# Performance work log

Hardware: AMD Instinct MI355X
Metric: run time of the kernel (lower is better)

The kernel has to match this reference:

```python
import jax, jax.numpy as jnp
import numpy as np

N, E, D, H, O = 100000, 1600000, 256, 128, 64


def setup_inputs() -> dict:
    key = jax.random.key(0)
    ks = jax.random.split(key, 10)
    x = jax.random.normal(ks[0], (N, D), dtype=jnp.float32)
    # edges without self loops (original adds remaining self loops itself)
    row = jax.random.randint(ks[1], (E,), 0, N)
    off = jax.random.randint(ks[2], (E,), 1, N)
    col = (row + off) % N
    edge_index = jnp.stack([row, col]).astype(jnp.int64)
    # positive PPMI edge weights (stand-in for cached random-walk PPMI values)
    ppmi_edge_weight = jax.random.uniform(ks[3], (E,), dtype=jnp.float32, minval=0.1, maxval=1.0)
    # glorot-style weights (shared between GCN and PPMI branches, as in the module)
    W1 = jax.random.normal(ks[4], (D, H), dtype=jnp.float32) * np.sqrt(2.0 / (D + H))
    b1 = jnp.zeros((H,), dtype=jnp.float32)
    W2 = jax.random.normal(ks[5], (H, O), dtype=jnp.float32) * np.sqrt(2.0 / (H + O))
    b2 = jnp.zeros((O,), dtype=jnp.float32)
    dense_w = jax.random.normal(ks[6], (O, 1), dtype=jnp.float32) * np.sqrt(2.0 / (O + 1))
    dense_b = jnp.zeros((1,), dtype=jnp.float32)
    return {"x": x, "edge_index": edge_index, "ppmi_edge_weight": ppmi_edge_weight,
            "W1": W1, "b1": b1, "W2": W2, "b2": b2,
            "dense_w": dense_w, "dense_b": dense_b}


def _sym_norm(row, col, ew, n):
    # deg^-0.5[row] * w * deg^-0.5[col], deg from scatter-add over source index
    deg = jax.ops.segment_sum(ew, row, num_segments=n)
    dis = jnp.where(deg > 0, deg ** -0.5, 0.0)
    return dis[row] * ew * dis[col]


def _gconv(h, W, b, row, col, norm, n):
    hw = h @ W                              # [N, F_out]
    msg = norm[:, None] * hw[row]           # gather + scale, [E', F_out]
    return jax.ops.segment_sum(msg, col, num_segments=n) + b


def reference(x, edge_index, ppmi_edge_weight, W1, b1, W2, b2, dense_w, dense_b):
    n = x.shape[0]
    row = edge_index[0].astype(jnp.int32)
    col = edge_index[1].astype(jnp.int32)
    sl = jnp.arange(n, dtype=jnp.int32)
    row_sl = jnp.concatenate([row, sl])
    col_sl = jnp.concatenate([col, sl])
    ones_sl = jnp.ones((n,), dtype=x.dtype)

    # GCN branch: edge_weight = 1, plus self loops (fill_value = 1)
    gcn_ew = jnp.concatenate([jnp.ones((row.shape[0],), dtype=x.dtype), ones_sl])
    gnorm = _sym_norm(row_sl, col_sl, gcn_ew, n)
    g = jax.nn.relu(_gconv(x, W1, b1, row_sl, col_sl, gnorm, n))  # dropout p in eval -> identity
    g = _gconv(g, W2, b2, row_sl, col_sl, gnorm, n)

    # PPMI branch: precomputed positive weights, plus self loops
    ppmi_ew = jnp.concatenate([ppmi_edge_weight.astype(x.dtype), ones_sl])
    pnorm = _sym_norm(row_sl, col_sl, ppmi_ew, n)
    p = jax.nn.relu(_gconv(x, W1, b1, row_sl, col_sl, pnorm, n))
    p = _gconv(p, W2, b2, row_sl, col_sl, pnorm, n)

    stacked = jnp.stack([g, p], axis=1)                 # [N, 2, O]
    logits = stacked @ dense_w + dense_b                # [N, 2, 1]
    w = jax.nn.softmax(logits, axis=1)
    return jnp.sum(stacked * w, axis=1)                 # [N, O]
```

## Files before the change

### kernel.cpp

```cpp
#include <hip/hip_runtime.h>
#include <hip/hip_bf16.h>
#include <math.h>

#define DD 256
#define HH 128
#define OO 64

#define EPB 8192
#define BKT 512
#define AWIN 512

typedef __attribute__((ext_vector_type(8))) __bf16 bf16x8;
typedef __attribute__((ext_vector_type(4))) __bf16 bf16x4;
typedef __attribute__((ext_vector_type(4))) float f32x4;
typedef __attribute__((ext_vector_type(2))) float f32x2;
typedef __attribute__((ext_vector_type(4))) int i32x4;

__device__ inline float2 bf2_to_f2(unsigned u) {
    float2 r;
    r.x = __uint_as_float(u << 16);
    r.y = __uint_as_float(u & 0xffff0000u);
    return r;
}

__global__ void part_count_kernel(const int* __restrict__ row, const int* __restrict__ col,
                                  int e, int nb,
                                  int* __restrict__ cnt_col, int* __restrict__ cnt_row) {
    __shared__ int hc[256], hr[256];
    int t = threadIdx.x;
    if (t < 256) { hc[t] = 0; hr[t] = 0; }
    __syncthreads();
    int base = blockIdx.x * EPB;
    int lim  = min(EPB, e - base);
    for (int i = t; i < lim; i += 512) {
        atomicAdd(&hc[col[base + i] >> 9], 1);
        atomicAdd(&hr[row[base + i] >> 9], 1);
    }
    __syncthreads();
    if (t < nb) {
        cnt_col[blockIdx.x * nb + t] = hc[t];
        cnt_row[blockIdx.x * nb + t] = hr[t];
    }
}

__global__ void scan_blocks_kernel(const int* __restrict__ cnt_col, const int* __restrict__ cnt_row,
                                   int* __restrict__ base_col, int* __restrict__ base_row,
                                   int* __restrict__ tot_col, int* __restrict__ tot_row,
                                   int nblk, int nb) {
    __shared__ int s[256];
    int side = (blockIdx.x >= (unsigned)nb) ? 1 : 0;
    int b = blockIdx.x - side * nb;
    const int* cnt = side ? cnt_row : cnt_col;
    int* base = side ? base_row : base_col;
    int* tot  = side ? tot_row  : tot_col;
    int t = threadIdx.x;
    int v = (t < nblk) ? cnt[(size_t)t * nb + b] : 0;
    s[t] = v;
    __syncthreads();
    for (int off = 1; off < 256; off <<= 1) {
        int u = (t >= off) ? s[t - off] : 0;
        __syncthreads();
        s[t] += u;
        __syncthreads();
    }
    if (t < nblk) base[(size_t)t * nb + b] = s[t] - v;
    if (t == 255) tot[b] = s[255];
}

__global__ void add_bases_kernel(int* __restrict__ base_col, int* __restrict__ base_row,
                                 const int* __restrict__ tot_col, const int* __restrict__ tot_row,
                                 int* __restrict__ bb_col, int* __restrict__ bb_row,
                                 int* __restrict__ row_ptr, int n, int e, int nblk, int nb) {
    __shared__ int s[256];
    __shared__ int bbv;
    int side = (blockIdx.x >= (unsigned)nb) ? 1 : 0;
    int b = blockIdx.x - side * nb;
    const int* tot = side ? tot_row : tot_col;
    int* base = side ? base_row : base_col;
    int t = threadIdx.x;
    int v = (t < nb) ? tot[t] : 0;
    s[t] = v;
    __syncthreads();
    for (int off = 1; off < 256; off <<= 1) {
        int u = (t >= off) ? s[t - off] : 0;
        __syncthreads();
        s[t] += u;
        __syncthreads();
    }
    if (t == 0) {
        bbv = (b > 0) ? s[b - 1] : 0;
        (side ? bb_row : bb_col)[b] = bbv;
    }
    __syncthreads();
    int add = bbv;
    for (int j = t; j < nblk; j += blockDim.x) base[(size_t)j * nb + b] += add;
    if (blockIdx.x == 0 && t == 0) row_ptr[n] = e;
}

__global__ void part_scatter_kernel(const int* __restrict__ row, const int* __restrict__ col,
                                    const float* __restrict__ ppmi,
                                    const int* __restrict__ base_col, const int* __restrict__ base_row,
                                    int4* __restrict__ tmp_col, int2* __restrict__ tmp_row,
                                    int e, int nb) {
    __shared__ int cc[256], cr[256];
    int t = threadIdx.x;
    if (t < nb) {
        cc[t] = base_col[blockIdx.x * nb + t];
        cr[t] = base_row[blockIdx.x * nb + t];
    }
    __syncthreads();
    int base = blockIdx.x * EPB;
    int lim  = min(EPB, e - base);
    for (int i = t; i < lim; i += 512) {
        int r = row[base + i], c = col[base + i];
        int w = __float_as_int(ppmi[base + i]);
        int sc = atomicAdd(&cc[c >> 9], 1);
        tmp_col[sc] = make_int4(c, r, w, 0);
        int sr = atomicAdd(&cr[r >> 9], 1);
        tmp_row[sr] = make_int2(r, w);
    }
}

__global__ void deg_bucket_kernel(const int2* __restrict__ tmp_row,
                                  const int* __restrict__ bb_row, const int* __restrict__ tot_row,
                                  float2* __restrict__ dis, int n) {
    __shared__ float dg[BKT], dp[BKT];
    int t = threadIdx.x;
    dg[t] = 1.0f; dp[t] = 1.0f;
    __syncthreads();
    int b = blockIdx.x;
    int beg = bb_row[b], cnt = tot_row[b];
    for (int i = t; i < cnt; i += 512) {
        int2 cell = tmp_row[beg + i];
        int lr = cell.x & (BKT - 1);
        atomicAdd(&dg[lr], 1.0f);
        atomicAdd(&dp[lr], __int_as_float(cell.y));
    }
    __syncthreads();
    int g = (b << 9) + t;
    if (g < n) dis[g] = make_float2(rsqrtf(dg[t]), rsqrtf(dp[t]));
}

__launch_bounds__(512)
__global__ void csr_bucket_kernel(const int4* __restrict__ tmp_col,
                                  const int* __restrict__ bb_col, const int* __restrict__ tot_col,
                                  const float2* __restrict__ dis,
                                  int* __restrict__ row_ptr, int4* __restrict__ csr_meta, int n) {
    __shared__ int hist[BKT], s[BKT], cur[BKT];
    int t = threadIdx.x;
    hist[t] = 0;
    __syncthreads();
    int b = blockIdx.x;
    int beg = bb_col[b], cnt = tot_col[b];
    for (int i = t; i < cnt; i += BKT) atomicAdd(&hist[tmp_col[beg + i].x & (BKT - 1)], 1);
    __syncthreads();
    int own = hist[t];
    s[t] = own;
    __syncthreads();
    for (int off = 1; off < BKT; off <<= 1) {
        int v = (t >= off) ? s[t - off] : 0;
        __syncthreads();
        s[t] += v;
        __syncthreads();
    }
    int gslot = beg + s[t] - own;
    cur[t] = gslot;
    int gc = (b << 9) + t;
    if (gc < n) row_ptr[gc] = gslot;
    __syncthreads();
    for (int i = t; i < cnt; i += BKT) {
        int4 cell = tmp_col[beg + i];
        int lc = cell.x & (BKT - 1);
        int slot = atomicAdd(&cur[lc], 1);
        int r = cell.y;
        float w = __int_as_float(cell.z);
        float2 d = dis[r];
        csr_meta[slot] = make_int4(r, __float_as_int(d.x), __float_as_int(d.y * w), 0);
    }
}

__global__ void conv_w_kernel(const float* __restrict__ W, __bf16* __restrict__ Bh,
                              __bf16* __restrict__ Bl, int K, int N) {
    int i = blockIdx.x * blockDim.x + threadIdx.x;
    if (i >= K * N) return;
    int k = i / N, nn = i % N;
    float v = W[i];
    __bf16 h = (__bf16)v;
    Bh[(size_t)nn * K + k] = h;
    Bl[(size_t)nn * K + k] = (__bf16)(v - (float)h);
}

template<int BM, int BN, typename OT, bool ILV>
__launch_bounds__(256, 2)
__global__ void mfma_gemm_kernel(const float* __restrict__ A,
                                 const __bf16* __restrict__ Bth, const __bf16* __restrict__ Btl,
                                 OT* __restrict__ C, int M, int K, int nHalf) {
    constexpr int BK  = 32;
    constexpr int LDK = BK + 8;
    constexpr int WM  = BM / 4;
    constexpr int MT  = WM / 16;
    constexpr int NT  = BN / 16;
    __shared__ __bf16 Ash[BM * LDK];
    __shared__ __bf16 Asl[BM * LDK];
    __shared__ __bf16 Bsh[BN * LDK];
    __shared__ __bf16 Bsl[BN * LDK];

    const int tid  = threadIdx.x;
    const int wave = tid >> 6;
    const int lane = tid & 63;
    const int quad = lane >> 4;
    const int l16  = lane & 15;
    const int row0 = blockIdx.x * BM;

    f32x4 acc[MT][NT] = {};

    for (int k0 = 0; k0 < K; k0 += BK) {
#pragma unroll
        for (int p = 0; p < BM / 32; ++p) {
            int lin = p * 256 + tid;
            int r   = lin >> 3;
            int kc  = (lin & 7) * 4;
            int gr  = row0 + r;
            float4 v;
            if (gr < M) v = *(const float4*)(A + (size_t)gr * K + k0 + kc);
            else        v = make_float4(0.f, 0.f, 0.f, 0.f);
            __bf16 h0 = (__bf16)v.x, h1 = (__bf16)v.y, h2 = (__bf16)v.z, h3 = (__bf16)v.w;
            __bf16 l0 = (__bf16)(v.x - (float)h0), l1 = (__bf16)(v.y - (float)h1);
            __bf16 l2 = (__bf16)(v.z - (float)h2), l3 = (__bf16)(v.w - (float)h3);
            *(bf16x4*)&Ash[r * LDK + kc] = (bf16x4){h0, h1, h2, h3};
            *(bf16x4*)&Asl[r * LDK + kc] = (bf16x4){l0, l1, l2, l3};
        }
#pragma unroll
        for (int p = 0; p < BN / 64; ++p) {
            int lin = p * 256 + tid;
            int r   = lin >> 2;
            int kc  = (lin & 3) * 8;
            *(uint4*)&Bsh[r * LDK + kc] = *(const uint4*)(Bth + (size_t)r * K + k0 + kc);
            *(uint4*)&Bsl[r * LDK + kc] = *(const uint4*)(Btl + (size_t)r * K + k0 + kc);
        }
        __syncthreads();

        bf16x8 bh[NT], bl[NT];
#pragma unroll
        for (int j = 0; j < NT; ++j) {
            bh[j] = *(const bf16x8*)&Bsh[(j * 16 + l16) * LDK + quad * 8];
            bl[j] = *(const bf16x8*)&Bsl[(j * 16 + l16) * LDK + quad * 8];
        }
#pragma unroll
        for (int i = 0; i < MT; ++i) {
            int m = wave * WM + i * 16 + l16;
            bf16x8 ah = *(const bf16x8*)&Ash[m * LDK + quad * 8];
            bf16x8 al = *(const bf16x8*)&Asl[m * LDK + quad * 8];
#pragma unroll
            for (int j = 0; j < NT; ++j) {
                acc[i][j] = __builtin_amdgcn_mfma_f32_16x16x32_bf16(ah, bh[j], acc[i][j], 0, 0, 0);
                acc[i][j] = __builtin_amdgcn_mfma_f32_16x16x32_bf16(ah, bl[j], acc[i][j], 0, 0, 0);
                acc[i][j] = __builtin_amdgcn_mfma_f32_16x16x32_bf16(al, bh[j], acc[i][j], 0, 0, 0);
            }
        }
        __syncthreads();
    }

#pragma unroll
    for (int i = 0; i < MT; ++i) {
#pragma unroll
        for (int rg = 0; rg < 4; ++rg) {
            int gr = row0 + wave * WM + i * 16 + quad * 4 + rg;
            if (gr < M) {
                if constexpr (ILV) {
                    int s = (gr >= nHalf) ? 1 : 0;
                    size_t base = (size_t)(gr - s * nHalf) * (BN * 2) + s;
#pragma unroll
                    for (int j = 0; j < NT; ++j)
                        C[base + (size_t)(j * 16 + l16) * 2] = (OT)acc[i][j][rg];
                } else {
#pragma unroll
                    for (int j = 0; j < NT; ++j)
                        C[(size_t)gr * BN + j * 16 + l16] = (OT)acc[i][j][rg];
                }
            }
        }
    }
}

__global__ void agg1_pull_kernel(const int* __restrict__ row_ptr, const int4* __restrict__ meta,
                                 const __bf16* __restrict__ hw1,
                                 const float2* __restrict__ dis,
                                 const float* __restrict__ b1,
                                 float* __restrict__ g_out, float* __restrict__ p_out, int n) {
    __shared__ i32x4 sm[AWIN];
    const int tid  = threadIdx.x;
    const int wave = tid >> 6;
    const int lane = tid & 63;
    const int c0   = blockIdx.x * 4;
    const int c    = c0 + wave;
    const int beg0 = row_ptr[c0];
    const int end3 = row_ptr[min(c0 + 4, n)];
    int beg = 0, end = 0;
    if (c < n) { beg = row_ptr[c]; end = row_ptr[c + 1]; }
    const int f2 = lane * 2;
    float sgx = 0.f, sgy = 0.f, spx = 0.f, spy = 0.f;

    for (int w = beg0; w < end3; w += AWIN) {
        const int cnt = min(AWIN, end3 - w);
        __syncthreads();
        for (int i = tid; i < cnt; i += 256)
            sm[i] = __builtin_nontemporal_load((const i32x4*)meta + w + i);
        __syncthreads();
        int t = max(beg, w);
        const int hi = min(end, w + cnt);
        for (; t + 8 <= hi; t += 8) {
            i32x4 m[8];
#pragma unroll
            for (int q = 0; q < 8; ++q) m[q] = sm[t - w + q];
            unsigned u[8];
#pragma unroll
            for (int q = 0; q < 8; ++q)
                u[q] = *(const unsigned*)(hw1 + ((size_t)(unsigned)m[q].x << 7) + f2);
#pragma unroll
            for (int q = 0; q < 8; ++q) {
                float2 h = bf2_to_f2(u[q]);
                float wg = __uint_as_float((unsigned)m[q].y);
                float wp = __uint_as_float((unsigned)m[q].z);
                sgx += wg * h.x; sgy += wg * h.y;
                spx += wp * h.x; spy += wp * h.y;
            }
        }
        if (t + 4 <= hi) {
            i32x4 m[4];
#pragma unroll
            for (int q = 0; q < 4; ++q) m[q] = sm[t - w + q];
            unsigned u[4];
#pragma unroll
            for (int q = 0; q < 4; ++q)
                u[q] = *(const unsigned*)(hw1 + ((size_t)(unsigned)m[q].x << 7) + f2);
#pragma unroll
            for (int q = 0; q < 4; ++q) {
                float2 h = bf2_to_f2(u[q]);
                float wg = __uint_as_float((unsigned)m[q].y);
                float wp = __uint_as_float((unsigned)m[q].z);
                sgx += wg * h.x; sgy += wg * h.y;
                spx += wp * h.x; spy += wp * h.y;
            }
            t += 4;
        }
        for (; t < hi; ++t) {
            i32x4 m0 = sm[t - w];
            float2 h0 = bf2_to_f2(*(const unsigned*)(hw1 + ((size_t)(unsigned)m0.x << 7) + f2));
            float wg0 = __uint_as_float((unsigned)m0.y);
            float wp0 = __uint_as_float((unsigned)m0.z);
            sgx += wg0 * h0.x; sgy += wg0 * h0.y;
            spx += wp0 * h0.x; spy += wp0 * h0.y;
        }
    }

    if (c < n) {
        float2 d = dis[c];
        size_t idx = ((size_t)c << 7) + f2;
        float2 hs = bf2_to_f2(*(const unsigned*)(hw1 + idx));
        float2 bv = *(const float2*)(b1 + f2);
        float gx = d.x * sgx + d.x * d.x * hs.x + bv.x;
        float gy = d.x * sgy + d.x * d.x * hs.y + bv.y;
        float px = d.y * spx + d.y * d.y * hs.x + bv.x;
        float py = d.y * spy + d.y * d.y * hs.y + bv.y;
        f32x2 go, po;
        go[0] = gx > 0.f ? gx : 0.f;  go[1] = gy > 0.f ? gy : 0.f;
        po[0] = px > 0.f ? px : 0.f;  po[1] = py > 0.f ? py : 0.f;
        __builtin_nontemporal_store(go, (f32x2*)(g_out + idx));
        __builtin_nontemporal_store(po, (f32x2*)(p_out + idx));
    }
}

__global__ void agg2_final_kernel(const int* __restrict__ row_ptr, const int4* __restrict__ meta,
                                  const __bf16* __restrict__ hw2i,
                                  const float2* __restrict__ dis,
                                  const float* __restrict__ b2,
                                  const float* __restrict__ dense_w, const float* __restrict__ dense_b,
                                  float* __restrict__ out, int n) {
    __shared__ i32x4 sm[AWIN];
    const int tid  = threadIdx.x;
    const int wave = tid >> 6;
    const int f    = tid & 63;
    const int c0   = blockIdx.x * 4;
    const int c    = c0 + wave;
    const int beg0 = row_ptr[c0];
    const int end3 = row_ptr[min(c0 + 4, n)];
    int beg = 0, end = 0;
    if (c < n) { beg = row_ptr[c]; end = row_ptr[c + 1]; }
    const int f2 = f * 2;
    float sg = 0.f, sp = 0.f;

    for (int w = beg0; w < end3; w += AWIN) {
        const int cnt = min(AWIN, end3 - w);
        __syncthreads();
        for (int i = tid; i < cnt; i += 256)
            sm[i] = __builtin_nontemporal_load((const i32x4*)meta + w + i);
        __syncthreads();
        int t = max(beg, w);
        const int hi = min(end, w + cnt);
        for (; t + 8 <= hi; t += 8) {
            i32x4 m[8];
#pragma unroll
            for (int q = 0; q < 8; ++q) m[q] = sm[t - w + q];
            unsigned u[8];
#pragma unroll
            for (int q = 0; q < 8; ++q)
                u[q] = *(const unsigned*)(hw2i + ((size_t)(unsigned)m[q].x << 7) + f2);
#pragma unroll
            for (int q = 0; q < 8; ++q) {
                float2 g0 = bf2_to_f2(u[q]);
                sg += __uint_as_float((unsigned)m[q].y) * g0.x;
                sp += __uint_as_float((unsigned)m[q].z) * g0.y;
            }
        }
        if (t + 4 <= hi) {
            i32x4 m[4];
#pragma unroll
            for (int q = 0; q < 4; ++q) m[q] = sm[t - w + q];
            unsigned u[4];
#pragma unroll
            for (int q = 0; q < 4; ++q)
                u[q] = *(const unsigned*)(hw2i + ((size_t)(unsigned)m[q].x << 7) + f2);
#pragma unroll
            for (int q = 0; q < 4; ++q) {
                float2 g0 = bf2_to_f2(u[q]);
                sg += __uint_as_float((unsigned)m[q].y) * g0.x;
                sp += __uint_as_float((unsigned)m[q].z) * g0.y;
            }
            t += 4;
        }
        for (; t < hi; ++t) {
            i32x4 m0 = sm[t - w];
            float2 g0 = bf2_to_f2(*(const unsigned*)(hw2i + ((size_t)(unsigned)m0.x << 7) + f2));
            sg += __uint_as_float((unsigned)m0.y) * g0.x;
            sp += __uint_as_float((unsigned)m0.z) * g0.y;
        }
    }

    if (c < n) {
        float2 d = dis[c];
        float2 gps = bf2_to_f2(*(const unsigned*)(hw2i + ((size_t)c << 7) + f2));
        float bb = b2[f];
        float gv = d.x * sg + d.x * d.x * gps.x + bb;
        float pv = d.y * sp + d.y * d.y * gps.y + bb;
        float dwv = dense_w[f];
        float lg = gv * dwv, lp = pv * dwv;
#pragma unroll
        for (int off = 32; off > 0; off >>= 1) {
            lg += __shfl_xor(lg, off, 64);
            lp += __shfl_xor(lp, off, 64);
        }
        lg += dense_b[0];
        lp += dense_b[0];
        float m  = fmaxf(lg, lp);
        float eg = expf(lg - m), ep = expf(lp - m);
        float wgt = eg / (eg + ep);
        __builtin_nontemporal_store(wgt * gv + (1.0f - wgt) * pv, out + (size_t)c * OO + f);
    }
}

extern "C" void kernel_launch(void* const* d_in, const int* in_sizes, int n_in,
                              void* d_out, int out_size, void* d_ws, size_t ws_size,
                              hipStream_t stream) {
    const float* x    = (const float*)d_in[0];
    const int*   ei   = (const int*)d_in[1];
    const float* ppmi = (const float*)d_in[2];
    const float* W1   = (const float*)d_in[3];
    const float* b1   = (const float*)d_in[4];
    const float* W2   = (const float*)d_in[5];
    const float* b2   = (const float*)d_in[6];
    const float* dw   = (const float*)d_in[7];
    const float* db   = (const float*)d_in[8];
    float* out = (float*)d_out;

    const int n = in_sizes[0] / DD;
    const int e = in_sizes[2];
    const int* row = ei;
    const int* col = ei + e;

    const int nb   = (n + BKT - 1) / BKT;
    const int nblk = (e + EPB - 1) / EPB;

    float* ws      = (float*)d_ws;
    float2* dis    = (float2*)ws;
    __bf16* hw1    = (__bf16*)(ws + 2 * (size_t)n);
    float* g1      = (float*)(hw1 + (size_t)n * HH);
    float* p1      = g1 + (size_t)n * HH;
    int4* csr_meta = (int4*)(p1 + (size_t)n * HH);
    __bf16* bt1h   = (__bf16*)(csr_meta + e);
    __bf16* bt1l   = bt1h + (size_t)DD * HH;
    __bf16* bt2h   = bt1l + (size_t)DD * HH;
    __bf16* bt2l   = bt2h + (size_t)HH * OO;
    int* row_ptr   = (int*)(bt2l + (size_t)HH * OO);
    int* cnt_col   = row_ptr + (n + 1);
    int* base_col  = cnt_col + (size_t)nblk * nb;
    int* cnt_row   = base_col + (size_t)nblk * nb;
    int* base_row  = cnt_row + (size_t)nblk * nb;
    int* bb_col    = base_row + (size_t)nblk * nb;
    int* tot_col   = bb_col + nb;
    int* bb_row    = tot_col + nb;
    int* tot_row   = bb_row + nb;
    int4* tmp_col  = (int4*)g1;
    int2* tmp_row  = (int2*)p1;
    __bf16* hw2i   = hw1;

    const int T = 256;

    part_count_kernel<<<nblk, 512, 0, stream>>>(row, col, e, nb, cnt_col, cnt_row);
    scan_blocks_kernel<<<2 * nb, T, 0, stream>>>(cnt_col, cnt_row, base_col, base_row,
                                                 tot_col, tot_row, nblk, nb);
    add_bases_kernel<<<2 * nb, T, 0, stream>>>(base_col, base_row, tot_col, tot_row,
                                               bb_col, bb_row, row_ptr, n, e, nblk, nb);
    part_scatter_kernel<<<nblk, 512, 0, stream>>>(row, col, ppmi, base_col, base_row,
                                                  tmp_col, tmp_row, e, nb);
    deg_bucket_kernel<<<nb, 512, 0, stream>>>(tmp_row, bb_row, tot_row, dis, n);
    csr_bucket_kernel<<<nb, BKT, 0, stream>>>(tmp_col, bb_col, tot_col, dis,
                                              row_ptr, csr_meta, n);

    conv_w_kernel<<<(DD * HH + T - 1) / T, T, 0, stream>>>(W1, bt1h, bt1l, DD, HH);
    conv_w_kernel<<<(HH * OO + T - 1) / T, T, 0, stream>>>(W2, bt2h, bt2l, HH, OO);

    mfma_gemm_kernel<128, HH, __bf16, false><<<(n + 127) / 128, 256, 0, stream>>>(
        x, bt1h, bt1l, hw1, n, DD, 0);
    agg1_pull_kernel<<<(n + 3) / 4, 256, 0, stream>>>(row_ptr, csr_meta, hw1, dis, b1, g1, p1, n);
    mfma_gemm_kernel<128, OO, __bf16, true><<<(2 * n + 127) / 128, 256, 0, stream>>>(
        g1, bt2h, bt2l, hw2i, 2 * n, HH, n);
    agg2_final_kernel<<<(n + 3) / 4, 256, 0, stream>>>(row_ptr, csr_meta, hw2i, dis,
                                                       b2, dw, db, out, n);
}
```

Baseline: 512.8 us.

## Load GEMM operands directly into registers, dropping LDS staging and barriers

The split-bf16 MFMA GEMM no longer stages A and B tiles through shared memory. Each wave now loads its own A rows and the B fragments straight from global memory into registers, converts A to hi/lo bf16 in registers, and runs the MFMAs with no __syncthreads. This removes LDS traffic and block-level barriers. In exchange, every wave re-reads the full B fragments from global/L2, and the A loads are strided per lane rather than fully coalesced.

After: 549.2 us. 1.07x slower.

```diff
diff --git a/kernel.cpp b/kernel.cpp
--- a/kernel.cpp
+++ b/kernel.cpp
@@ -190,67 +190,48 @@
     Bl[(size_t)nn * K + k] = (__bf16)(v - (float)h);
 }
 
-template<int BM, int BN, typename OT, bool ILV>
+template<int BN, typename OT, bool ILV>
 __launch_bounds__(256, 2)
-__global__ void mfma_gemm_kernel(const float* __restrict__ A,
-                                 const __bf16* __restrict__ Bth, const __bf16* __restrict__ Btl,
-                                 OT* __restrict__ C, int M, int K, int nHalf) {
-    constexpr int BK  = 32;
-    constexpr int LDK = BK + 8;
-    constexpr int WM  = BM / 4;
-    constexpr int MT  = WM / 16;
-    constexpr int NT  = BN / 16;
-    __shared__ __bf16 Ash[BM * LDK];
-    __shared__ __bf16 Asl[BM * LDK];
-    __shared__ __bf16 Bsh[BN * LDK];
-    __shared__ __bf16 Bsl[BN * LDK];
-
+__global__ void mfma_gemm_reg_kernel(const float* __restrict__ A,
+                                     const __bf16* __restrict__ Bth, const __bf16* __restrict__ Btl,
+                                     OT* __restrict__ C, int M, int K, int nHalf) {
+    constexpr int NT = BN / 16;
     const int tid  = threadIdx.x;
     const int wave = tid >> 6;
     const int lane = tid & 63;
     const int quad = lane >> 4;
     const int l16  = lane & 15;
-    const int row0 = blockIdx.x * BM;
-
-    f32x4 acc[MT][NT] = {};
-
-    for (int k0 = 0; k0 < K; k0 += BK) {
-#pragma unroll
-        for (int p = 0; p < BM / 32; ++p) {
-            int lin = p * 256 + tid;
-            int r   = lin >> 3;
-            int kc  = (lin & 7) * 4;
-            int gr  = row0 + r;
-            float4 v;
-            if (gr < M) v = *(const float4*)(A + (size_t)gr * K + k0 + kc);
-            else        v = make_float4(0.f, 0.f, 0.f, 0.f);
-            __bf16 h0 = (__bf16)v.x, h1 = (__bf16)v.y, h2 = (__bf16)v.z, h3 = (__bf16)v.w;
-            __bf16 l0 = (__bf16)(v.x - (float)h0), l1 = (__bf16)(v.y - (float)h1);
-            __bf16 l2 = (__bf16)(v.z - (float)h2), l3 = (__bf16)(v.w - (float)h3);
-            *(bf16x4*)&Ash[r * LDK + kc] = (bf16x4){h0, h1, h2, h3};
-            *(bf16x4*)&Asl[r * LDK + kc] = (bf16x4){l0, l1, l2, l3};
-        }
-#pragma unroll
-        for (int p = 0; p < BN / 64; ++p) {
-            int lin = p * 256 + tid;
-            int r   = lin >> 2;
-            int kc  = (lin & 3) * 8;
-            *(uint4*)&Bsh[r * LDK + kc] = *(const uint4*)(Bth + (size_t)r * K + k0 + kc);
-            *(uint4*)&Bsl[r * LDK + kc] = *(const uint4*)(Btl + (size_t)r * K + k0 + kc);
-        }
-        __syncthreads();
-
+    const int row0 = blockIdx.x * 128 + wave * 32;
+
+    f32x4 acc[2][NT] = {};
+
+    for (int k0 = 0; k0 < K; k0 += 32) {
         bf16x8 bh[NT], bl[NT];
 #pragma unroll
         for (int j = 0; j < NT; ++j) {
-            bh[j] = *(const bf16x8*)&Bsh[(j * 16 + l16) * LDK + quad * 8];
-            bl[j] = *(const bf16x8*)&Bsl[(j * 16 + l16) * LDK + quad * 8];
-        }
-#pragma unroll
-        for (int i = 0; i < MT; ++i) {
-            int m = wave * WM + i * 16 + l16;
-            bf16x8 ah = *(const bf16x8*)&Ash[m * LDK + quad * 8];
-            bf16x8 al = *(const bf16x8*)&Asl[m * LDK + quad * 8];
+            size_t boff = (size_t)(j * 16 + l16) * K + k0 + quad * 8;
+            bh[j] = *(const bf16x8*)(Bth + boff);
+            bl[j] = *(const bf16x8*)(Btl + boff);
+        }
+#pragma unroll
+        for (int i = 0; i < 2; ++i) {
+            int gr = row0 + i * 16 + l16;
+            float4 v0 = make_float4(0.f, 0.f, 0.f, 0.f);
+            float4 v1 = make_float4(0.f, 0.f, 0.f, 0.f);
+            if (gr < M) {
+                const float* ap = A + (size_t)gr * K + k0 + quad * 8;
+                v0 = *(const float4*)ap;
+                v1 = *(const float4*)(ap + 4);
+            }
+            float vv0 = v0.x, vv1 = v0.y, vv2 = v0.z, vv3 = v0.w;
+            float vv4 = v1.x, vv5 = v1.y, vv6 = v1.z, vv7 = v1.w;
+            __bf16 h0 = (__bf16)vv0, h1 = (__bf16)vv1, h2 = (__bf16)vv2, h3 = (__bf16)vv3;
+            __bf16 h4 = (__bf16)vv4, h5 = (__bf16)vv5, h6 = (__bf16)vv6, h7 = (__bf16)vv7;
+            bf16x8 ah = (bf16x8){h0, h1, h2, h3, h4, h5, h6, h7};
+            bf16x8 al = (bf16x8){(__bf16)(vv0 - (float)h0), (__bf16)(vv1 - (float)h1),
+                                 (__bf16)(vv2 - (float)h2), (__bf16)(vv3 - (float)h3),
+                                 (__bf16)(vv4 - (float)h4), (__bf16)(vv5 - (float)h5),
+                                 (__bf16)(vv6 - (float)h6), (__bf16)(vv7 - (float)h7)};
 #pragma unroll
             for (int j = 0; j < NT; ++j) {
                 acc[i][j] = __builtin_amdgcn_mfma_f32_16x16x32_bf16(ah, bh[j], acc[i][j], 0, 0, 0);
@@ -258,14 +239,13 @@
                 acc[i][j] = __builtin_amdgcn_mfma_f32_16x16x32_bf16(al, bh[j], acc[i][j], 0, 0, 0);
             }
         }
-        __syncthreads();
-    }
-
-#pragma unroll
-    for (int i = 0; i < MT; ++i) {
+    }
+
+#pragma unroll
+    for (int i = 0; i < 2; ++i) {
 #pragma unroll
         for (int rg = 0; rg < 4; ++rg) {
-            int gr = row0 + wave * WM + i * 16 + quad * 4 + rg;
+            int gr = row0 + i * 16 + quad * 4 + rg;
             if (gr < M) {
                 if constexpr (ILV) {
                     int s = (gr >= nHalf) ? 1 : 0;
@@ -520,10 +500,10 @@
     conv_w_kernel<<<(DD * HH + T - 1) / T, T, 0, stream>>>(W1, bt1h, bt1l, DD, HH);
     conv_w_kernel<<<(HH * OO + T - 1) / T, T, 0, stream>>>(W2, bt2h, bt2l, HH, OO);
 
-    mfma_gemm_kernel<128, HH, __bf16, false><<<(n + 127) / 128, 256, 0, stream>>>(
+    mfma_gemm_reg_kernel<HH, __bf16, false><<<(n + 127) / 128, 256, 0, stream>>>(
         x, bt1h, bt1l, hw1, n, DD, 0);
     agg1_pull_kernel<<<(n + 3) / 4, 256, 0, stream>>>(row_ptr, csr_meta, hw1, dis, b1, g1, p1, n);
-    mfma_gemm_kernel<128, OO, __bf16, true><<<(2 * n + 127) / 128, 256, 0, stream>>>(
+    mfma_gemm_reg_kernel<OO, __bf16, true><<<(2 * n + 127) / 128, 256, 0, stream>>>(
         g1, bt2h, bt2l, hw2i, 2 * n, HH, n);
     agg2_final_kernel<<<(n + 3) / 4, 256, 0, stream>>>(row_ptr, csr_meta, hw2i, dis,
                                                        b2, dw, db, out, n);
```
